# Kernel tuning notes

Measured on AMD Instinct MI355X. Metric: run time of the kernel, lower is better.

## Reference

```python
import jax, jax.numpy as jnp
import numpy as np

N = 16384        # genes
N_REG = 8192     # regulons (rows of adj)
D_MODEL = 256
OUT_DIM = 128
ALPHA = 0.2      # leaky relu slope
NEG_INF = -9e15  # matches float(-9000000000000000.0)


def setup_inputs() -> dict:
    key = jax.random.key(0)
    k1, k2, k3, k4 = jax.random.split(key, 4)
    inp = jax.random.normal(k1, (N, D_MODEL), dtype=jnp.float32)
    adj = jax.random.randint(k2, (N_REG, N), 0, 2).astype(jnp.float32)
    # xavier_uniform with gain=1.414
    def xavier(k, shape, gain=1.414):
        fan_in, fan_out = shape[0], shape[1]
        a = gain * np.sqrt(6.0 / (fan_in + fan_out))
        return jax.random.uniform(k, shape, jnp.float32, -a, a)
    weights = xavier(k3, (D_MODEL, OUT_DIM))
    a_values = xavier(k4, (2 * OUT_DIM, 1))
    return {"input": inp, "adj_mat": adj, "weights": weights, "a_values": a_values}


def reference(input, adj_mat, weights, a_values):
    out_dim = weights.shape[1]
    n_reg = adj_mat.shape[0]
    w_h = input @ weights                                   # [N, out_dim]
    w_h1 = w_h[:n_reg] @ a_values[:out_dim]                 # [n_reg, 1]
    w_h2 = w_h @ a_values[out_dim:]                         # [N, 1]
    e = jax.nn.leaky_relu(w_h1 + w_h2.T, negative_slope=ALPHA)  # [n_reg, N]
    # masked attention: zero where adj==0, multiply by adj, fill zeros with -9e15
    att = jnp.where(adj_mat != 0, e, jnp.zeros_like(e)) * adj_mat
    att = jnp.where(att == 0, jnp.float32(NEG_INF), att)
    att = jax.nn.softmax(att, axis=1)
    # dropout is identity in eval mode (training=False)
    result = att @ w_h                                      # [n_reg, out_dim]
    return jax.nn.elu(result)                               # concat=True -> ELU
```

## Files before the change

kernel.cpp:

```cpp
#include <hip/hip_runtime.h>
#include <hip/hip_bf16.h>

typedef __bf16 bf16x8 __attribute__((ext_vector_type(8)));
typedef float  f32x4  __attribute__((ext_vector_type(4)));

#define NGENE  16384
#define NREG   8192
#define DMODEL 256
#define ODIM   128
#define KSPLIT 8
#define KCHUNK (NGENE / KSPLIT)
#define NSTEP  (KCHUNK / 32)
#define ALPHA  0.2f

__device__ __forceinline__ float bf2f(unsigned short u) {
  union { unsigned int i; float f; } v; v.i = ((unsigned int)u) << 16; return v.f;
}
__device__ __forceinline__ unsigned short f2bf(float f) {
  __bf16 b = (__bf16)f;
  return __builtin_bit_cast(unsigned short, b);
}
__device__ __forceinline__ void gl_lds16(const void* g, void* l) {
  __builtin_amdgcn_global_load_lds(
      (const __attribute__((address_space(1))) unsigned int*)g,
      (__attribute__((address_space(3))) unsigned int*)l, 16, 0, 0);
}

__global__ void k_detect(const unsigned int* __restrict__ adj_raw,
                         int* __restrict__ flag) {
  if (threadIdx.x == 0 && blockIdx.x == 0) {
    int isbf16 = 0;
    for (int i = 0; i < 256; ++i)
      if ((adj_raw[i] & 0xffffu) == 0x3f80u) isbf16 = 1;
    *flag = isbf16;
  }
}

__global__ void k_wt(const void* __restrict__ W, const void* __restrict__ AVin,
                     const int* __restrict__ flag,
                     unsigned short* __restrict__ WT,
                     float* __restrict__ AVf) {
  const int n = blockIdx.x, k = threadIdx.x;
  const int bf = *flag;
  float w = bf ? bf2f(((const unsigned short*)W)[k * ODIM + n])
               : ((const float*)W)[k * ODIM + n];
  WT[n * DMODEL + k] = f2bf(w);
  if (n == 0)
    AVf[k] = bf ? bf2f(((const unsigned short*)AVin)[k]) : ((const float*)AVin)[k];
}

__global__ __launch_bounds__(256) void k_wh(
    const void* __restrict__ X, const int* __restrict__ flag,
    const unsigned short* __restrict__ WT, const float* __restrict__ AVf,
    unsigned short* __restrict__ WhT,
    float* __restrict__ w1, float* __restrict__ w2) {
  __shared__ float lds[4][16][ODIM + 1];
  const int tid = threadIdx.x;
  const int w = tid >> 6, l = tid & 63;
  const int q = l >> 4, ln = l & 15;
  const int m0 = blockIdx.x * 64 + w * 16;

  f32x4 acc[8];
#pragma unroll
  for (int t = 0; t < 8; ++t) acc[t] = (f32x4){0.f, 0.f, 0.f, 0.f};

  const int bf = *flag;
#pragma unroll
  for (int ks = 0; ks < 8; ++ks) {
    const int k0 = ks * 32 + q * 8;
    bf16x8 a;
    if (bf) {
      a = *(const bf16x8*)((const unsigned short*)X + (size_t)(m0 + ln) * DMODEL + k0);
    } else {
      const float* xp = (const float*)X + (size_t)(m0 + ln) * DMODEL + k0;
      f32x4 x0 = *(const f32x4*)xp, x1 = *(const f32x4*)(xp + 4);
#pragma unroll
      for (int j = 0; j < 8; ++j) a[j] = (__bf16)((j < 4) ? x0[j] : x1[j - 4]);
    }
#pragma unroll
    for (int t = 0; t < 8; ++t) {
      bf16x8 b = *(const bf16x8*)(WT + (size_t)(16 * t + ln) * DMODEL + k0);
      acc[t] = __builtin_amdgcn_mfma_f32_16x16x32_bf16(a, b, acc[t], 0, 0, 0);
    }
  }

  float a1v[8], a2v[8];
#pragma unroll
  for (int t = 0; t < 8; ++t) {
    a1v[t] = AVf[16 * t + ln];
    a2v[t] = AVf[ODIM + 16 * t + ln];
  }
#pragma unroll
  for (int r = 0; r < 4; ++r) {
    float s1 = 0.f, s2 = 0.f;
#pragma unroll
    for (int t = 0; t < 8; ++t) {
      s1 += acc[t][r] * a1v[t];
      s2 += acc[t][r] * a2v[t];
    }
    s1 += __shfl_xor(s1, 1); s1 += __shfl_xor(s1, 2);
    s1 += __shfl_xor(s1, 4); s1 += __shfl_xor(s1, 8);
    s2 += __shfl_xor(s2, 1); s2 += __shfl_xor(s2, 2);
    s2 += __shfl_xor(s2, 4); s2 += __shfl_xor(s2, 8);
    const int row = m0 + q * 4 + r;
    if (ln == 0) {
      w2[row] = s2;
      if (row < NREG) w1[row] = s1;
    }
  }

#pragma unroll
  for (int t = 0; t < 8; ++t)
#pragma unroll
    for (int r = 0; r < 4; ++r)
      lds[w][q * 4 + r][16 * t + ln] = acc[t][r];
  __syncthreads();

#pragma unroll
  for (int rr = 0; rr < 2; ++rr) {
    const int n = 2 * l + rr;
    unsigned short oh[16];
#pragma unroll
    for (int m = 0; m < 16; ++m) oh[m] = f2bf(lds[w][m][n]);
    uint4* dh = (uint4*)(WhT + (size_t)n * NGENE + m0);
    dh[0] = ((uint4*)oh)[0]; dh[1] = ((uint4*)oh)[1];
  }
}

__device__ __forceinline__ void att_compute(
    const float* av0, const float* av1, const float* w2v,
    const unsigned char* lsb, int q, int ln, float w1v0, float w1v1,
    f32x4* acc0, f32x4* acc1, float& ssum0, float& ssum1) {
  bf16x8 af0, af1;
#pragma unroll
  for (int j = 0; j < 8; ++j) {
    float s0 = w1v0 + w2v[j];
    float p0 = av0[j] * __expf(fmaxf(s0, ALPHA * s0));
    __bf16 pb0 = (__bf16)p0;
    af0[j] = pb0; ssum0 += (float)pb0;
    float s1 = w1v1 + w2v[j];
    float p1 = av1[j] * __expf(fmaxf(s1, ALPHA * s1));
    __bf16 pb1 = (__bf16)p1;
    af1[j] = pb1; ssum1 += (float)pb1;
  }
#pragma unroll
  for (int t = 0; t < 8; ++t) {
    int n = 16 * t + ln;
    int s = n * 4 + (q ^ ((n >> 1) & 3));
    bf16x8 b = *(const bf16x8*)(lsb + s * 16);
    acc0[t] = __builtin_amdgcn_mfma_f32_16x16x32_bf16(af0, b, acc0[t], 0, 0, 0);
    acc1[t] = __builtin_amdgcn_mfma_f32_16x16x32_bf16(af1, b, acc1[t], 0, 0, 0);
  }
}

__global__ __launch_bounds__(256) void k_att(
    const void* __restrict__ adj, const int* __restrict__ flag,
    const unsigned short* __restrict__ WhT,
    const float* __restrict__ w1, const float* __restrict__ w2,
    float* __restrict__ Opart, float* __restrict__ Spart) {
  __shared__ __align__(16) unsigned char ls[2][8192];
  const int tid = threadIdx.x;
  const int w = tid >> 6, l = tid & 63;
  const int q = l >> 4, ln = l & 15;
  const int mb = blockIdx.x & 63;
  const int kc = blockIdx.x >> 6;
  const int m0 = mb * 128 + w * 32;
  const int r0 = m0 + ln, r1 = m0 + 16 + ln;
  const int kbase = kc * KCHUNK;

  const float w1v0 = w1[r0], w1v1 = w1[r1];

  size_t soff[2];
  int ldsoff[2];
#pragma unroll
  for (int i = 0; i < 2; ++i) {
    int s = i * 256 + tid;
    int n = s >> 2;
    int qs = (s & 3) ^ ((n >> 1) & 3);
    soff[i] = (size_t)n * NGENE + qs * 8;
    ldsoff[i] = (i * 256 + w * 64) * 16;
  }
  auto stage = [&](int kglob, int buf) {
#pragma unroll
    for (int i = 0; i < 2; ++i)
      gl_lds16(WhT + soff[i] + kglob, &ls[buf][ldsoff[i]]);
  };

  f32x4 acc0[8], acc1[8];
#pragma unroll
  for (int t = 0; t < 8; ++t) {
    acc0[t] = (f32x4){0.f, 0.f, 0.f, 0.f};
    acc1[t] = (f32x4){0.f, 0.f, 0.f, 0.f};
  }
  float ssum0 = 0.f, ssum1 = 0.f;
  const float* wp = w2 + kbase + q * 8;

  stage(kbase, 0);

  if (*flag) {
    const unsigned short* A = (const unsigned short*)adj;
    const unsigned short* ap0 = A + (size_t)r0 * NGENE + kbase + q * 8;
    const unsigned short* ap1 = A + (size_t)r1 * NGENE + kbase + q * 8;
    uint4 c0 = *(const uint4*)ap0;
    uint4 c1 = *(const uint4*)ap1;
    f32x4 wa = *(const f32x4*)wp, wb = *(const f32x4*)(wp + 4);
    for (int st = 0; st < NSTEP; ++st) {
      __syncthreads();
      if (st + 1 < NSTEP) stage(kbase + (st + 1) * 32, (st + 1) & 1);
      uint4 u0 = c0, u1 = c1; f32x4 va = wa, vb = wb;
      if (st + 1 < NSTEP) {
        c0 = *(const uint4*)(ap0 + (st + 1) * 32);
        c1 = *(const uint4*)(ap1 + (st + 1) * 32);
        wa = *(const f32x4*)(wp + (st + 1) * 32);
        wb = *(const f32x4*)(wp + (st + 1) * 32 + 4);
      }
      float av0[8], av1[8], w2v[8];
      const unsigned int* p0w = (const unsigned int*)&u0;
      const unsigned int* p1w = (const unsigned int*)&u1;
#pragma unroll
      for (int j = 0; j < 8; ++j) {
        union { unsigned int i; float f; } x, y;
        x.i = (j & 1) ? (p0w[j >> 1] & 0xffff0000u) : (p0w[j >> 1] << 16);
        y.i = (j & 1) ? (p1w[j >> 1] & 0xffff0000u) : (p1w[j >> 1] << 16);
        av0[j] = x.f; av1[j] = y.f;
        w2v[j] = (j < 4) ? va[j] : vb[j - 4];
      }
      att_compute(av0, av1, w2v, ls[st & 1], q, ln, w1v0, w1v1,
                  acc0, acc1, ssum0, ssum1);
    }
  } else {
    const float* A = (const float*)adj;
    const float* ap0 = A + (size_t)r0 * NGENE + kbase + q * 8;
    const float* ap1 = A + (size_t)r1 * NGENE + kbase + q * 8;
    f32x4 c0a = *(const f32x4*)ap0, c0b = *(const f32x4*)(ap0 + 4);
    f32x4 c1a = *(const f32x4*)ap1, c1b = *(const f32x4*)(ap1 + 4);
    f32x4 wa = *(const f32x4*)wp, wb = *(const f32x4*)(wp + 4);
    for (int st = 0; st < NSTEP; ++st) {
      __syncthreads();
      if (st + 1 < NSTEP) stage(kbase + (st + 1) * 32, (st + 1) & 1);
      f32x4 u0a = c0a, u0b = c0b, u1a = c1a, u1b = c1b;
      f32x4 va = wa, vb = wb;
      if (st + 1 < NSTEP) {
        c0a = *(const f32x4*)(ap0 + (st + 1) * 32);
        c0b = *(const f32x4*)(ap0 + (st + 1) * 32 + 4);
        c1a = *(const f32x4*)(ap1 + (st + 1) * 32);
        c1b = *(const f32x4*)(ap1 + (st + 1) * 32 + 4);
        wa = *(const f32x4*)(wp + (st + 1) * 32);
        wb = *(const f32x4*)(wp + (st + 1) * 32 + 4);
      }
      float av0[8], av1[8], w2v[8];
#pragma unroll
      for (int j = 0; j < 8; ++j) {
        av0[j] = (j < 4) ? u0a[j] : u0b[j - 4];
        av1[j] = (j < 4) ? u1a[j] : u1b[j - 4];
        w2v[j] = (j < 4) ? va[j] : vb[j - 4];
      }
      att_compute(av0, av1, w2v, ls[st & 1], q, ln, w1v0, w1v1,
                  acc0, acc1, ssum0, ssum1);
    }
  }

  ssum0 += __shfl_xor(ssum0, 16); ssum0 += __shfl_xor(ssum0, 32);
  ssum1 += __shfl_xor(ssum1, 16); ssum1 += __shfl_xor(ssum1, 32);
  if (l < 16) {
    Spart[(size_t)kc * NREG + r0] = ssum0;
    Spart[(size_t)kc * NREG + r1] = ssum1;
  }
  float* op0 = Opart + ((size_t)kc * NREG + m0) * ODIM;
  float* op1 = op0 + 16 * ODIM;
#pragma unroll
  for (int t = 0; t < 8; ++t)
#pragma unroll
    for (int r = 0; r < 4; ++r) {
      op0[(q * 4 + r) * ODIM + 16 * t + ln] = acc0[t][r];
      op1[(q * 4 + r) * ODIM + 16 * t + ln] = acc1[t][r];
    }
}

__global__ void k_red(const float* __restrict__ Opart,
                      const float* __restrict__ Spart,
                      const int* __restrict__ flag, void* __restrict__ out) {
  const int id = blockIdx.x * 256 + threadIdx.x;
  const int row = id >> 7;
  float o = 0.f, s = 0.f;
#pragma unroll
  for (int k = 0; k < KSPLIT; ++k) {
    o += Opart[(size_t)k * (NREG * ODIM) + id];
    s += Spart[(size_t)k * NREG + row];
  }
  const float r = o / s;
  const float res = r > 0.f ? r : (__expf(r) - 1.f);
  if (*flag) ((unsigned short*)out)[id] = f2bf(res);
  else       ((float*)out)[id] = res;
}

extern "C" void kernel_launch(void* const* d_in, const int* in_sizes, int n_in,
                              void* d_out, int out_size, void* d_ws, size_t ws_size,
                              hipStream_t stream) {
  const void* X   = d_in[0];
  const void* ADJ = d_in[1];
  const void* W   = d_in[2];
  const void* AV  = d_in[3];

  char* ws = (char*)d_ws;
  size_t off = 0;
  auto alloc = [&](size_t bytes) -> void* {
    void* p = ws + off; off += (bytes + 255) & ~(size_t)255; return p;
  };
  unsigned short* WhT = (unsigned short*)alloc((size_t)ODIM * NGENE * 2);
  unsigned short* WT  = (unsigned short*)alloc((size_t)DMODEL * ODIM * 2);
  float* AVf   = (float*)alloc(2 * ODIM * 4);
  float* w1    = (float*)alloc((size_t)NREG * 4);
  float* w2    = (float*)alloc((size_t)NGENE * 4);
  int*   flag  = (int*)alloc(256);
  float* Spart = (float*)alloc((size_t)KSPLIT * NREG * 4);
  float* Opart = (float*)alloc((size_t)KSPLIT * NREG * ODIM * 4);

  hipLaunchKernelGGL(k_detect, dim3(1), dim3(64), 0, stream,
                     (const unsigned int*)ADJ, flag);
  hipLaunchKernelGGL(k_wt, dim3(ODIM), dim3(DMODEL), 0, stream,
                     W, AV, flag, WT, AVf);
  hipLaunchKernelGGL(k_wh, dim3(NGENE / 64), dim3(256), 0, stream,
                     X, flag, WT, AVf, WhT, w1, w2);
  hipLaunchKernelGGL(k_att, dim3(64 * KSPLIT), dim3(256), 0, stream,
                     ADJ, flag, WhT, w1, w2, Opart, Spart);
  hipLaunchKernelGGL(k_red, dim3((NREG * ODIM) / 256), dim3(256), 0, stream,
                     Opart, Spart, flag, d_out);
}
```

Baseline: 760.0 us.

## Load WhT B-fragments directly from global, drop LDS staging and barriers

```diff
diff --git a/kernel.cpp b/kernel.cpp
--- a/kernel.cpp
+++ b/kernel.cpp
@@ -20,20 +20,14 @@
   __bf16 b = (__bf16)f;
   return __builtin_bit_cast(unsigned short, b);
 }
-__device__ __forceinline__ void gl_lds16(const void* g, void* l) {
-  __builtin_amdgcn_global_load_lds(
-      (const __attribute__((address_space(1))) unsigned int*)g,
-      (__attribute__((address_space(3))) unsigned int*)l, 16, 0, 0);
-}
 
 __global__ void k_detect(const unsigned int* __restrict__ adj_raw,
                          int* __restrict__ flag) {
-  if (threadIdx.x == 0 && blockIdx.x == 0) {
-    int isbf16 = 0;
-    for (int i = 0; i < 256; ++i)
-      if ((adj_raw[i] & 0xffffu) == 0x3f80u) isbf16 = 1;
-    *flag = isbf16;
-  }
+  int found = 0;
+  for (int i = threadIdx.x; i < 1024; i += 64)
+    if ((adj_raw[i] & 0xffffu) == 0x3f80u) found = 1;
+  int any = __any(found) ? 1 : 0;
+  if (threadIdx.x == 0) *flag = any;
 }
 
 __global__ void k_wt(const void* __restrict__ W, const void* __restrict__ AVin,
@@ -127,38 +121,11 @@
   }
 }
 
-__device__ __forceinline__ void att_compute(
-    const float* av0, const float* av1, const float* w2v,
-    const unsigned char* lsb, int q, int ln, float w1v0, float w1v1,
-    f32x4* acc0, f32x4* acc1, float& ssum0, float& ssum1) {
-  bf16x8 af0, af1;
-#pragma unroll
-  for (int j = 0; j < 8; ++j) {
-    float s0 = w1v0 + w2v[j];
-    float p0 = av0[j] * __expf(fmaxf(s0, ALPHA * s0));
-    __bf16 pb0 = (__bf16)p0;
-    af0[j] = pb0; ssum0 += (float)pb0;
-    float s1 = w1v1 + w2v[j];
-    float p1 = av1[j] * __expf(fmaxf(s1, ALPHA * s1));
-    __bf16 pb1 = (__bf16)p1;
-    af1[j] = pb1; ssum1 += (float)pb1;
-  }
-#pragma unroll
-  for (int t = 0; t < 8; ++t) {
-    int n = 16 * t + ln;
-    int s = n * 4 + (q ^ ((n >> 1) & 3));
-    bf16x8 b = *(const bf16x8*)(lsb + s * 16);
-    acc0[t] = __builtin_amdgcn_mfma_f32_16x16x32_bf16(af0, b, acc0[t], 0, 0, 0);
-    acc1[t] = __builtin_amdgcn_mfma_f32_16x16x32_bf16(af1, b, acc1[t], 0, 0, 0);
-  }
-}
-
-__global__ __launch_bounds__(256) void k_att(
+__global__ __launch_bounds__(256, 2) void k_att(
     const void* __restrict__ adj, const int* __restrict__ flag,
     const unsigned short* __restrict__ WhT,
     const float* __restrict__ w1, const float* __restrict__ w2,
     float* __restrict__ Opart, float* __restrict__ Spart) {
-  __shared__ __align__(16) unsigned char ls[2][8192];
   const int tid = threadIdx.x;
   const int w = tid >> 6, l = tid & 63;
   const int q = l >> 4, ln = l & 15;
@@ -170,21 +137,10 @@
 
   const float w1v0 = w1[r0], w1v1 = w1[r1];
 
-  size_t soff[2];
-  int ldsoff[2];
-#pragma unroll
-  for (int i = 0; i < 2; ++i) {
-    int s = i * 256 + tid;
-    int n = s >> 2;
-    int qs = (s & 3) ^ ((n >> 1) & 3);
-    soff[i] = (size_t)n * NGENE + qs * 8;
-    ldsoff[i] = (i * 256 + w * 64) * 16;
-  }
-  auto stage = [&](int kglob, int buf) {
-#pragma unroll
-    for (int i = 0; i < 2; ++i)
-      gl_lds16(WhT + soff[i] + kglob, &ls[buf][ldsoff[i]]);
-  };
+  const unsigned short* bpt[8];
+#pragma unroll
+  for (int t = 0; t < 8; ++t)
+    bpt[t] = WhT + (size_t)(16 * t + ln) * NGENE + kbase + q * 8;
 
   f32x4 acc0[8], acc1[8];
 #pragma unroll
@@ -194,27 +150,36 @@
   }
   float ssum0 = 0.f, ssum1 = 0.f;
   const float* wp = w2 + kbase + q * 8;
-
-  stage(kbase, 0);
 
   if (*flag) {
     const unsigned short* A = (const unsigned short*)adj;
     const unsigned short* ap0 = A + (size_t)r0 * NGENE + kbase + q * 8;
     const unsigned short* ap1 = A + (size_t)r1 * NGENE + kbase + q * 8;
-    uint4 c0 = *(const uint4*)ap0;
-    uint4 c1 = *(const uint4*)ap1;
-    f32x4 wa = *(const f32x4*)wp, wb = *(const f32x4*)(wp + 4);
+    uint4 c0[2], c1[2]; f32x4 wa[2], wb[2];
+#pragma unroll
+    for (int i = 0; i < 2; ++i) {
+      c0[i] = *(const uint4*)(ap0 + i * 32);
+      c1[i] = *(const uint4*)(ap1 + i * 32);
+      wa[i] = *(const f32x4*)(wp + i * 32);
+      wb[i] = *(const f32x4*)(wp + i * 32 + 4);
+    }
+#pragma unroll 2
     for (int st = 0; st < NSTEP; ++st) {
-      __syncthreads();
-      if (st + 1 < NSTEP) stage(kbase + (st + 1) * 32, (st + 1) & 1);
-      uint4 u0 = c0, u1 = c1; f32x4 va = wa, vb = wb;
-      if (st + 1 < NSTEP) {
-        c0 = *(const uint4*)(ap0 + (st + 1) * 32);
-        c1 = *(const uint4*)(ap1 + (st + 1) * 32);
-        wa = *(const f32x4*)(wp + (st + 1) * 32);
-        wb = *(const f32x4*)(wp + (st + 1) * 32 + 4);
-      }
-      float av0[8], av1[8], w2v[8];
+      const int cur = st & 1;
+      uint4 u0 = c0[cur], u1 = c1[cur];
+      f32x4 va = wa[cur], vb = wb[cur];
+      if (st + 2 < NSTEP) {
+        c0[cur] = *(const uint4*)(ap0 + (st + 2) * 32);
+        c1[cur] = *(const uint4*)(ap1 + (st + 2) * 32);
+        wa[cur] = *(const f32x4*)(wp + (st + 2) * 32);
+        wb[cur] = *(const f32x4*)(wp + (st + 2) * 32 + 4);
+      }
+      bf16x8 bv[8];
+#pragma unroll
+      for (int t = 0; t < 8; ++t)
+        bv[t] = *(const bf16x8*)(bpt[t] + st * 32);
+
+      bf16x8 af0, af1;
       const unsigned int* p0w = (const unsigned int*)&u0;
       const unsigned int* p1w = (const unsigned int*)&u1;
 #pragma unroll
@@ -222,41 +187,74 @@
         union { unsigned int i; float f; } x, y;
         x.i = (j & 1) ? (p0w[j >> 1] & 0xffff0000u) : (p0w[j >> 1] << 16);
         y.i = (j & 1) ? (p1w[j >> 1] & 0xffff0000u) : (p1w[j >> 1] << 16);
-        av0[j] = x.f; av1[j] = y.f;
-        w2v[j] = (j < 4) ? va[j] : vb[j - 4];
-      }
-      att_compute(av0, av1, w2v, ls[st & 1], q, ln, w1v0, w1v1,
-                  acc0, acc1, ssum0, ssum1);
+        const float w2v = (j < 4) ? va[j] : vb[j - 4];
+        float s0 = w1v0 + w2v;
+        float p0 = x.f * __expf(fmaxf(s0, ALPHA * s0));
+        __bf16 pb0 = (__bf16)p0;
+        af0[j] = pb0; ssum0 += (float)pb0;
+        float s1 = w1v1 + w2v;
+        float p1 = y.f * __expf(fmaxf(s1, ALPHA * s1));
+        __bf16 pb1 = (__bf16)p1;
+        af1[j] = pb1; ssum1 += (float)pb1;
+      }
+#pragma unroll
+      for (int t = 0; t < 8; ++t) {
+        acc0[t] = __builtin_amdgcn_mfma_f32_16x16x32_bf16(af0, bv[t], acc0[t], 0, 0, 0);
+        acc1[t] = __builtin_amdgcn_mfma_f32_16x16x32_bf16(af1, bv[t], acc1[t], 0, 0, 0);
+      }
     }
   } else {
     const float* A = (const float*)adj;
     const float* ap0 = A + (size_t)r0 * NGENE + kbase + q * 8;
     const float* ap1 = A + (size_t)r1 * NGENE + kbase + q * 8;
-    f32x4 c0a = *(const f32x4*)ap0, c0b = *(const f32x4*)(ap0 + 4);
-    f32x4 c1a = *(const f32x4*)ap1, c1b = *(const f32x4*)(ap1 + 4);
-    f32x4 wa = *(const f32x4*)wp, wb = *(const f32x4*)(wp + 4);
+    f32x4 c0a[2], c0b[2], c1a[2], c1b[2], wa[2], wb[2];
+#pragma unroll
+    for (int i = 0; i < 2; ++i) {
+      c0a[i] = *(const f32x4*)(ap0 + i * 32);
+      c0b[i] = *(const f32x4*)(ap0 + i * 32 + 4);
+      c1a[i] = *(const f32x4*)(ap1 + i * 32);
+      c1b[i] = *(const f32x4*)(ap1 + i * 32 + 4);
+      wa[i] = *(const f32x4*)(wp + i * 32);
+      wb[i] = *(const f32x4*)(wp + i * 32 + 4);
+    }
+#pragma unroll 2
     for (int st = 0; st < NSTEP; ++st) {
-      __syncthreads();
-      if (st + 1 < NSTEP) stage(kbase + (st + 1) * 32, (st + 1) & 1);
-      f32x4 u0a = c0a, u0b = c0b, u1a = c1a, u1b = c1b;
-      f32x4 va = wa, vb = wb;
-      if (st + 1 < NSTEP) {
-        c0a = *(const f32x4*)(ap0 + (st + 1) * 32);
-        c0b = *(const f32x4*)(ap0 + (st + 1) * 32 + 4);
-        c1a = *(const f32x4*)(ap1 + (st + 1) * 32);
-        c1b = *(const f32x4*)(ap1 + (st + 1) * 32 + 4);
-        wa = *(const f32x4*)(wp + (st + 1) * 32);
-        wb = *(const f32x4*)(wp + (st + 1) * 32 + 4);
-      }
-      float av0[8], av1[8], w2v[8];
+      const int cur = st & 1;
+      f32x4 u0a = c0a[cur], u0b = c0b[cur], u1a = c1a[cur], u1b = c1b[cur];
+      f32x4 va = wa[cur], vb = wb[cur];
+      if (st + 2 < NSTEP) {
+        c0a[cur] = *(const f32x4*)(ap0 + (st + 2) * 32);
+        c0b[cur] = *(const f32x4*)(ap0 + (st + 2) * 32 + 4);
+        c1a[cur] = *(const f32x4*)(ap1 + (st + 2) * 32);
+        c1b[cur] = *(const f32x4*)(ap1 + (st + 2) * 32 + 4);
+        wa[cur] = *(const f32x4*)(wp + (st + 2) * 32);
+        wb[cur] = *(const f32x4*)(wp + (st + 2) * 32 + 4);
+      }
+      bf16x8 bv[8];
+#pragma unroll
+      for (int t = 0; t < 8; ++t)
+        bv[t] = *(const bf16x8*)(bpt[t] + st * 32);
+
+      bf16x8 af0, af1;
 #pragma unroll
       for (int j = 0; j < 8; ++j) {
-        av0[j] = (j < 4) ? u0a[j] : u0b[j - 4];
-        av1[j] = (j < 4) ? u1a[j] : u1b[j - 4];
-        w2v[j] = (j < 4) ? va[j] : vb[j - 4];
-      }
-      att_compute(av0, av1, w2v, ls[st & 1], q, ln, w1v0, w1v1,
-                  acc0, acc1, ssum0, ssum1);
+        const float a0 = (j < 4) ? u0a[j] : u0b[j - 4];
+        const float a1 = (j < 4) ? u1a[j] : u1b[j - 4];
+        const float w2v = (j < 4) ? va[j] : vb[j - 4];
+        float s0 = w1v0 + w2v;
+        float p0 = a0 * __expf(fmaxf(s0, ALPHA * s0));
+        __bf16 pb0 = (__bf16)p0;
+        af0[j] = pb0; ssum0 += (float)pb0;
+        float s1 = w1v1 + w2v;
+        float p1 = a1 * __expf(fmaxf(s1, ALPHA * s1));
+        __bf16 pb1 = (__bf16)p1;
+        af1[j] = pb1; ssum1 += (float)pb1;
+      }
+#pragma unroll
+      for (int t = 0; t < 8; ++t) {
+        acc0[t] = __builtin_amdgcn_mfma_f32_16x16x32_bf16(af0, bv[t], acc0[t], 0, 0, 0);
+        acc1[t] = __builtin_amdgcn_mfma_f32_16x16x32_bf16(af1, bv[t], acc1[t], 0, 0, 0);
+      }
     }
   }
 
```

New measurement: 815.3 us. +7.3%, slower.
